# Optimization experiments

Measured on AMD Instinct MI355X. Metric: run time of the kernel, lower is better.

## Reference

```python
import jax, jax.numpy as jnp
import numpy as np

N, IN, HID, OUT, HEADS, E = 50000, 256, 128, 128, 2, 800000
NEG_SLOPE = 0.2


def gat_conv(x, edge_src, edge_dst, W, att_src, att_dst, bias):
    # x: [N, F_in]; W: [F_in, H*C]; att_*: [H, C]; bias: [C]
    n = x.shape[0]
    H, C = att_src.shape
    xl = (x @ W).reshape(n, H, C)                       # [N, H, C]
    a_src = jnp.sum(xl * att_src, axis=-1)              # [N, H]
    a_dst = jnp.sum(xl * att_dst, axis=-1)              # [N, H]
    e = jax.nn.leaky_relu(a_src[edge_src] + a_dst[edge_dst], NEG_SLOPE)  # [E+N, H]
    e_max = jax.ops.segment_max(e, edge_dst, num_segments=n)            # [N, H]
    e = jnp.exp(e - e_max[edge_dst])
    denom = jax.ops.segment_sum(e, edge_dst, num_segments=n)            # [N, H]
    alpha = e / (denom[edge_dst] + 1e-16)                               # [E+N, H]
    msg = xl[edge_src] * alpha[:, :, None]                              # [E+N, H, C]
    out = jax.ops.segment_sum(msg, edge_dst, num_segments=n)            # [N, H, C]
    return out.mean(axis=1) + bias                                      # concat=False: head mean


def setup_inputs() -> dict:
    key = jax.random.key(0)
    ks = jax.random.split(key, 12)
    x = jax.random.normal(ks[0], (N, IN), dtype=jnp.float32)
    edge_index = jax.random.randint(ks[1], (2, E), 0, N, dtype=jnp.int64)
    s = 0.1
    W0 = jax.random.normal(ks[2], (IN, HEADS * HID), dtype=jnp.float32) * s
    att_src0 = jax.random.normal(ks[3], (HEADS, HID), dtype=jnp.float32) * s
    att_dst0 = jax.random.normal(ks[4], (HEADS, HID), dtype=jnp.float32) * s
    bias0 = jnp.zeros((HID,), dtype=jnp.float32)
    W1 = jax.random.normal(ks[5], (HID, HEADS * HID), dtype=jnp.float32) * s
    att_src1 = jax.random.normal(ks[6], (HEADS, HID), dtype=jnp.float32) * s
    att_dst1 = jax.random.normal(ks[7], (HEADS, HID), dtype=jnp.float32) * s
    bias1 = jnp.zeros((HID,), dtype=jnp.float32)
    proj_w = jax.random.normal(ks[8], (HID, OUT), dtype=jnp.float32) * s
    proj_b = jnp.zeros((OUT,), dtype=jnp.float32)
    return {"x": x, "edge_index": edge_index,
            "W0": W0, "att_src0": att_src0, "att_dst0": att_dst0, "bias0": bias0,
            "W1": W1, "att_src1": att_src1, "att_dst1": att_dst1, "bias1": bias1,
            "proj_w": proj_w, "proj_b": proj_b}


def reference(x, edge_index, W0, att_src0, att_dst0, bias0, W1, att_src1, att_dst1, bias1, proj_w, proj_b):
    n = x.shape[0]
    loops = jnp.arange(n, dtype=edge_index.dtype)
    # PyG GATConv default add_self_loops=True
    src = jnp.concatenate([edge_index[0], loops])
    dst = jnp.concatenate([edge_index[1], loops])
    h = gat_conv(x, src, dst, W0, att_src0, att_dst0, bias0)
    h = jax.nn.gelu(h, approximate=False)
    h = gat_conv(h, src, dst, W1, att_src1, att_dst1, bias1)
    h = jax.nn.gelu(h, approximate=False)
    return h @ proj_w + proj_b
```

## Files before the change

### kernel.cpp

```cpp
#include <hip/hip_runtime.h>
#include <math.h>


#define NEG_SLOPE 0.2f

typedef __attribute__((ext_vector_type(8))) short bf16x8;
typedef __attribute__((ext_vector_type(8))) ushort u16x8;
typedef __attribute__((ext_vector_type(4))) float f32x4;

__device__ __forceinline__ void split_f32(float x, ushort& h, ushort& l)
{
    unsigned b = __float_as_uint(x);
    h = (ushort)(b >> 16);
    float xh = __uint_as_float(b & 0xffff0000u);
    l = (ushort)(__float_as_uint(x - xh) >> 16);
}

__device__ __forceinline__ ushort f32_to_bf16_rne(float x)
{
    unsigned u = __float_as_uint(x);
    return (ushort)((u + 0x7fffu + ((u >> 16) & 1u)) >> 16);
}

__device__ __forceinline__ float bf16_to_f32(ushort u)
{
    return __uint_as_float(((unsigned)u) << 16);
}

__device__ __forceinline__ float lrelu(float x)
{
    return x > 0.f ? x : NEG_SLOPE * x;
}

__device__ __forceinline__ float gelu_exact(float x)
{
    return 0.5f * x * (1.0f + erff(x * 0.7071067811865476f));
}

__global__ __launch_bounds__(256)
void split_all_w(const float* __restrict__ W0, const float* __restrict__ W1,
                 const float* __restrict__ PW,
                 ushort* __restrict__ w0h, ushort* __restrict__ w0l,
                 ushort* __restrict__ w1h, ushort* __restrict__ w1l,
                 ushort* __restrict__ pwh, ushort* __restrict__ pwl)
{
    int t = blockIdx.x * 256 + threadIdx.x;
    ushort h, l;
    if (t < 65536) {
        int k = t >> 8, n = t & 255;
        split_f32(W0[t], h, l);
        w0h[n * 256 + k] = h; w0l[n * 256 + k] = l;
    } else if (t < 65536 + 32768) {
        int u = t - 65536;
        int k = u >> 8, n = u & 255;
        split_f32(W1[u], h, l);
        w1h[n * 128 + k] = h; w1l[n * 128 + k] = l;
    } else if (t < 65536 + 32768 + 16384) {
        int u = t - 65536 - 32768;
        int k = u >> 7, n = u & 127;
        split_f32(PW[u], h, l);
        pwh[n * 128 + k] = h; pwl[n * 128 + k] = l;
    }
}

__global__ __launch_bounds__(256)
void watt_prep_kernel(const float* __restrict__ W,
                      const float* __restrict__ att_s,
                      const float* __restrict__ att_d,
                      float* __restrict__ watt,
                      int C, int Nout)
{
    const int k = blockIdx.x;
    const int t = threadIdx.x;
    const int h = t >> 7, c = t & 127;
    const int lane = t & 63, wid = t >> 6;

    float ps = 0.f, pd = 0.f;
    if (c < C) {
        const float w = W[(size_t)k * Nout + h * C + c];
        ps = w * att_s[h * C + c];
        pd = w * att_d[h * C + c];
    }
#pragma unroll
    for (int off = 1; off < 64; off <<= 1) {
        ps += __shfl_xor(ps, off, 64);
        pd += __shfl_xor(pd, off, 64);
    }
    __shared__ float sm[4][2];
    if (lane == 0) { sm[wid][0] = ps; sm[wid][1] = pd; }
    __syncthreads();
    if (t == 0) {
        watt[k * 4 + 0] = sm[0][0] + sm[1][0];
        watt[k * 4 + 1] = sm[2][0] + sm[3][0];
        watt[k * 4 + 2] = sm[0][1] + sm[1][1];
        watt[k * 4 + 3] = sm[2][1] + sm[3][1];
    }
}

__global__ __launch_bounds__(256)
void attn_matvec_kernel(const float* __restrict__ X,
                        const float* __restrict__ watt,
                        float* __restrict__ a_s, float* __restrict__ a_d,
                        int n, int K)
{
    const int wave = threadIdx.x >> 6;
    const int lane = threadIdx.x & 63;
    const int v = blockIdx.x * 4 + wave;
    if (v >= n) return;

    float s0 = 0.f, s1 = 0.f, d0 = 0.f, d1 = 0.f;
    const int k0 = lane << 2;
    if (k0 < K) {
        const float4 xv = *(const float4*)(X + (size_t)v * K + k0);
        const float x4[4] = {xv.x, xv.y, xv.z, xv.w};
#pragma unroll
        for (int i = 0; i < 4; ++i) {
            const float4 wv = *(const float4*)(watt + (k0 + i) * 4);
            s0 += x4[i] * wv.x;
            s1 += x4[i] * wv.y;
            d0 += x4[i] * wv.z;
            d1 += x4[i] * wv.w;
        }
    }
#pragma unroll
    for (int off = 1; off < 64; off <<= 1) {
        s0 += __shfl_xor(s0, off, 64);
        s1 += __shfl_xor(s1, off, 64);
        d0 += __shfl_xor(d0, off, 64);
        d1 += __shfl_xor(d1, off, 64);
    }
    if (lane == 0) {
        *(float2*)(a_s + (size_t)v * 2) = make_float2(s0, s1);
        *(float2*)(a_d + (size_t)v * 2) = make_float2(d0, d1);
    }
}

template<int BN, bool SPLITA>
__global__ __launch_bounds__(512)
void mfma_gemm3(const float* __restrict__ Af,
                const ushort* __restrict__ Aio,
                const ushort* __restrict__ Bth, const ushort* __restrict__ Btl,
                const float* __restrict__ bias,
                float* __restrict__ Cf, ushort* __restrict__ Cb,
                int M, int K)
{
    constexpr int NF = BN / 64;
    __shared__ ushort Ah[4][128][8];
    __shared__ ushort Al[4][128][8];
    __shared__ ushort Bh[4][BN][8];
    __shared__ ushort Bl[4][BN][8];

    const int tid = threadIdx.x;
    const int r0 = blockIdx.x * 128;
    const int w = tid >> 6, lane = tid & 63;
    const int wr = (w & 1) * 64;
    const int wc = (w >> 1) * (BN / 4);
    const int lr = lane & 15, kb = lane >> 4;

    const int arow = tid >> 2;
    const int apl = tid & 3;

    f32x4 acc[4][NF] = {};

    for (int kk = 0; kk < K; kk += 32) {
        {
            const int row = r0 + arow;
            u16x8 h0 = {}, l0 = {};
            if (row < M) {
                if constexpr (SPLITA) {
                    const float* p = Af + (size_t)row * K + kk + apl * 8;
                    float4 v0 = *(const float4*)(p);
                    float4 v1 = *(const float4*)(p + 4);
                    float va[8] = {v0.x, v0.y, v0.z, v0.w, v1.x, v1.y, v1.z, v1.w};
#pragma unroll
                    for (int i = 0; i < 8; ++i) {
                        ushort hh_, ll_;
                        split_f32(va[i], hh_, ll_);
                        h0[i] = hh_; l0[i] = ll_;
                    }
                } else {
                    const ushort* p = Aio + (size_t)row * (2 * K) + kk + apl * 8;
                    h0 = *(const u16x8*)(p);
                    l0 = *(const u16x8*)(p + K);
                }
            }
            *(u16x8*)&Ah[apl][arow][0] = h0;
            *(u16x8*)&Al[apl][arow][0] = l0;
        }
        if constexpr (BN == 256) {
            const int col = tid >> 1, half = tid & 1;
            const ushort* ph = Bth + (size_t)col * K + kk + half * 16;
            const ushort* pl = Btl + (size_t)col * K + kk + half * 16;
            *(u16x8*)&Bh[half * 2 + 0][col][0] = *(const u16x8*)(ph);
            *(u16x8*)&Bh[half * 2 + 1][col][0] = *(const u16x8*)(ph + 8);
            *(u16x8*)&Bl[half * 2 + 0][col][0] = *(const u16x8*)(pl);
            *(u16x8*)&Bl[half * 2 + 1][col][0] = *(const u16x8*)(pl + 8);
        } else {
            const int col = tid >> 2, pl = tid & 3;
            *(u16x8*)&Bh[pl][col][0] = *(const u16x8*)(Bth + (size_t)col * K + kk + pl * 8);
            *(u16x8*)&Bl[pl][col][0] = *(const u16x8*)(Btl + (size_t)col * K + kk + pl * 8);
        }
        __syncthreads();

        bf16x8 ah[4], al[4];
#pragma unroll
        for (int m = 0; m < 4; ++m) {
            ah[m] = *(const bf16x8*)&Ah[kb][wr + m * 16 + lr][0];
            al[m] = *(const bf16x8*)&Al[kb][wr + m * 16 + lr][0];
        }
#pragma unroll
        for (int n = 0; n < NF; ++n) {
            const bf16x8 bh = *(const bf16x8*)&Bh[kb][wc + n * 16 + lr][0];
            const bf16x8 bl = *(const bf16x8*)&Bl[kb][wc + n * 16 + lr][0];
#pragma unroll
            for (int m = 0; m < 4; ++m) {
                acc[m][n] = __builtin_amdgcn_mfma_f32_16x16x32_bf16(ah[m], bh, acc[m][n], 0, 0, 0);
                acc[m][n] = __builtin_amdgcn_mfma_f32_16x16x32_bf16(ah[m], bl, acc[m][n], 0, 0, 0);
                acc[m][n] = __builtin_amdgcn_mfma_f32_16x16x32_bf16(al[m], bh, acc[m][n], 0, 0, 0);
            }
        }
        __syncthreads();
    }

#pragma unroll
    for (int n = 0; n < NF; ++n) {
        const int col = wc + n * 16 + lr;
        const float bv = bias ? bias[col] : 0.f;
#pragma unroll
        for (int m = 0; m < 4; ++m) {
            const int rowb = r0 + wr + m * 16 + kb * 4;
#pragma unroll
            for (int j = 0; j < 4; ++j) {
                const int row = rowb + j;
                if (row < M) {
                    const float val = acc[m][n][j] + bv;
                    if (Cf) Cf[(size_t)row * BN + col] = val;
                    if (Cb) Cb[(size_t)row * BN + col] = f32_to_bf16_rne(val);
                }
            }
        }
    }
}

__global__ __launch_bounds__(256)
void edge_alpha_kernel(const float* __restrict__ a_s,
                       const float* __restrict__ a_d,
                       const int* __restrict__ rowptr,
                       const int* __restrict__ esrc,
                       float* __restrict__ walpha,
                       float* __restrict__ nodeP,
                       int n)
{
    const int wave = threadIdx.x >> 6;
    const int lane = threadIdx.x & 63;
    const int v = blockIdx.x * 4 + wave;
    if (v >= n) return;
    const int h = lane >> 5;
    const int j0 = lane & 31;

    const float adv = a_d[v * 2 + h];
    const float e0 = lrelu(a_s[v * 2 + h] + adv);
    const int beg = rowptr[v], end = rowptr[v + 1];

    float m = e0;
    for (int i = beg + j0; i < end; i += 32) {
        const int src = esrc[i];
        m = fmaxf(m, lrelu(a_s[src * 2 + h] + adv));
    }
#pragma unroll
    for (int off = 1; off < 32; off <<= 1)
        m = fmaxf(m, __shfl_xor(m, off, 64));

    float ssum = (j0 == 0) ? __expf(e0 - m) : 0.f;
    for (int i = beg + j0; i < end; i += 32) {
        const int src = esrc[i];
        const float wgt = __expf(lrelu(a_s[src * 2 + h] + adv) - m);
        walpha[(size_t)i * 2 + h] = wgt;
        ssum += wgt;
    }
#pragma unroll
    for (int off = 1; off < 32; off <<= 1)
        ssum += __shfl_xor(ssum, off, 64);

    if (j0 == 0) {
        float2 p;
        p.x = __expf(e0 - m);
        p.y = 1.0f / (ssum + 1e-16f);
        *(float2*)(nodeP + (size_t)v * 4 + h * 2) = p;
    }
}

__global__ __launch_bounds__(256)
void gat_gather_kernel(const ushort* __restrict__ xlb,
                       const int* __restrict__ rowptr,
                       const int* __restrict__ esrc,
                       const float* __restrict__ walpha,
                       const float* __restrict__ nodeP,
                       const float* __restrict__ bias,
                       const float* __restrict__ watt,
                       float* __restrict__ a_s, float* __restrict__ a_d,
                       ushort* __restrict__ outio,
                       int n)
{
    const int wave = threadIdx.x >> 6;
    const int lane = threadIdx.x & 63;
    const int v = blockIdx.x * 4 + wave;
    if (v >= n) return;
    const int h = lane >> 5;
    const int j0 = lane & 31;
    const int c4 = j0 << 2;

    const float2 p = *(const float2*)(nodeP + (size_t)v * 4 + h * 2);
    const ushort4 xv4 = *(const ushort4*)(xlb + (size_t)v * 256 + (lane << 2));
    float4 acc0, acc1;
    acc0.x = p.x * bf16_to_f32(xv4.x);
    acc0.y = p.x * bf16_to_f32(xv4.y);
    acc0.z = p.x * bf16_to_f32(xv4.z);
    acc0.w = p.x * bf16_to_f32(xv4.w);
    acc1 = make_float4(0.f, 0.f, 0.f, 0.f);

    const int beg = rowptr[v], end = rowptr[v + 1];
    for (int i = beg; i < end; i += 32) {
        const int cnt = min(32, end - i);
        int myidx = 0;
        float myw = 0.f;
        if (j0 < cnt) {
            myidx = esrc[i + j0];
            myw = walpha[(size_t)(i + j0) * 2 + h];
        }
#pragma unroll 2
        for (int j = 0; j < cnt; ++j) {
            const int src = __builtin_amdgcn_readlane(myidx, j);
            const float wgt = __shfl(myw, j, 32);
            const ushort4 xs4 = *(const ushort4*)(xlb + (size_t)src * 256 + (lane << 2));
            if (j & 1) {
                acc1.x += wgt * bf16_to_f32(xs4.x);
                acc1.y += wgt * bf16_to_f32(xs4.y);
                acc1.z += wgt * bf16_to_f32(xs4.z);
                acc1.w += wgt * bf16_to_f32(xs4.w);
            } else {
                acc0.x += wgt * bf16_to_f32(xs4.x);
                acc0.y += wgt * bf16_to_f32(xs4.y);
                acc0.z += wgt * bf16_to_f32(xs4.z);
                acc0.w += wgt * bf16_to_f32(xs4.w);
            }
        }
    }

    float4 r;
    r.x = (acc0.x + acc1.x) * p.y;
    r.y = (acc0.y + acc1.y) * p.y;
    r.z = (acc0.z + acc1.z) * p.y;
    r.w = (acc0.w + acc1.w) * p.y;
    float4 o;
    o.x = 0.5f * (r.x + __shfl_xor(r.x, 32, 64));
    o.y = 0.5f * (r.y + __shfl_xor(r.y, 32, 64));
    o.z = 0.5f * (r.z + __shfl_xor(r.z, 32, 64));
    o.w = 0.5f * (r.w + __shfl_xor(r.w, 32, 64));

    const float4 bb = *(const float4*)(bias + c4);
    o.x = gelu_exact(o.x + bb.x);
    o.y = gelu_exact(o.y + bb.y);
    o.z = gelu_exact(o.z + bb.z);
    o.w = gelu_exact(o.w + bb.w);

    if (watt) {
        const float ov[4] = {o.x, o.y, o.z, o.w};
        float s0 = 0.f, s1 = 0.f, d0 = 0.f, d1 = 0.f;
#pragma unroll
        for (int i = 0; i < 4; ++i) {
            const float4 wv = *(const float4*)(watt + (c4 + i) * 4);
            s0 += ov[i] * wv.x;
            s1 += ov[i] * wv.y;
            d0 += ov[i] * wv.z;
            d1 += ov[i] * wv.w;
        }
#pragma unroll
        for (int off = 1; off < 64; off <<= 1) {
            s0 += __shfl_xor(s0, off, 64);
            s1 += __shfl_xor(s1, off, 64);
            d0 += __shfl_xor(d0, off, 64);
            d1 += __shfl_xor(d1, off, 64);
        }
        if (lane == 0) {
            *(float2*)(a_s + (size_t)v * 2) = make_float2(0.5f * s0, 0.5f * s1);
            *(float2*)(a_d + (size_t)v * 2) = make_float2(0.5f * d0, 0.5f * d1);
        }
    }

    ushort4 st;
    ushort hh_, ll_;
    split_f32(o.x, hh_, ll_); st.x = (lane < 32) ? hh_ : ll_;
    split_f32(o.y, hh_, ll_); st.y = (lane < 32) ? hh_ : ll_;
    split_f32(o.z, hh_, ll_); st.z = (lane < 32) ? hh_ : ll_;
    split_f32(o.w, hh_, ll_); st.w = (lane < 32) ? hh_ : ll_;
    *(ushort4*)(outio + (size_t)v * 256 + (lane << 2)) = st;
}

__global__ __launch_bounds__(256)
void hist_kernel(const int* __restrict__ ei, int* __restrict__ cnt, int E)
{
    int e = blockIdx.x * 256 + threadIdx.x;
    if (e < E) atomicAdd(&cnt[ei[E + e]], 1);
}

__global__ __launch_bounds__(256)
void blocksum_kernel(const int* __restrict__ cnt, int* __restrict__ bsum, int n)
{
    __shared__ int sm[256];
    const int t = threadIdx.x;
    const int i = blockIdx.x * 256 + t;
    sm[t] = (i < n) ? cnt[i] : 0;
    __syncthreads();
#pragma unroll
    for (int off = 1; off < 256; off <<= 1) {
        int u = (t >= off) ? sm[t - off] : 0;
        __syncthreads();
        sm[t] += u;
        __syncthreads();
    }
    if (t == 255) bsum[blockIdx.x] = sm[255];
}

__global__ __launch_bounds__(256)
void scan_bsum_kernel(int* __restrict__ bsum, int nb, int* __restrict__ ptr, int n)
{
    __shared__ int sm[256];
    const int t = threadIdx.x;
    const int v = (t < nb) ? bsum[t] : 0;
    sm[t] = v;
    __syncthreads();
#pragma unroll
    for (int off = 1; off < 256; off <<= 1) {
        int u = (t >= off) ? sm[t - off] : 0;
        __syncthreads();
        sm[t] += u;
        __syncthreads();
    }
    if (t < nb) bsum[t] = sm[t] - v;
    if (t == 255) ptr[n] = sm[255];
}

__global__ __launch_bounds__(256)
void scan_out_kernel(const int* __restrict__ cnt, const int* __restrict__ bsum,
                     int* __restrict__ ptr, int* __restrict__ pcur, int n)
{
    __shared__ int sm[256];
    const int t = threadIdx.x;
    const int i = blockIdx.x * 256 + t;
    const int v = (i < n) ? cnt[i] : 0;
    sm[t] = v;
    __syncthreads();
#pragma unroll
    for (int off = 1; off < 256; off <<= 1) {
        int u = (t >= off) ? sm[t - off] : 0;
        __syncthreads();
        sm[t] += u;
        __syncthreads();
    }
    if (i < n) {
        const int val = bsum[blockIdx.x] + sm[t] - v;
        ptr[i] = val;
        pcur[i] = val;
    }
}

__global__ __launch_bounds__(256)
void scatter_kernel(const int* __restrict__ ei, int* __restrict__ pcur,
                    int* __restrict__ esrc, int E)
{
    int e = blockIdx.x * 256 + threadIdx.x;
    if (e < E) {
        int dst = ei[E + e];
        int src = ei[e];
        int pos = atomicAdd(&pcur[dst], 1);
        esrc[pos] = src;
    }
}

extern "C" void kernel_launch(void* const* d_in, const int* in_sizes, int n_in,
                              void* d_out, int out_size, void* d_ws, size_t ws_size,
                              hipStream_t stream)
{
    const float* x       = (const float*)d_in[0];
    const int*   ei      = (const int*)d_in[1];
    const float* W0      = (const float*)d_in[2];
    const float* att_s0  = (const float*)d_in[3];
    const float* att_d0  = (const float*)d_in[4];
    const float* b0      = (const float*)d_in[5];
    const float* W1      = (const float*)d_in[6];
    const float* att_s1  = (const float*)d_in[7];
    const float* att_d1  = (const float*)d_in[8];
    const float* b1      = (const float*)d_in[9];
    const float* pw      = (const float*)d_in[10];
    const float* pb      = (const float*)d_in[11];

    const int N = in_sizes[0] / 256;
    const int E = in_sizes[1] / 2;
    const int NB = (N + 255) / 256;

    ushort* xlb = (ushort*)d_ws;
    ushort* hio = xlb + (size_t)N * 256;
    float*  a_s = (float*)(hio + (size_t)N * 256);
    float*  a_d = a_s + (size_t)N * 2;
    float*  wal = a_d + (size_t)N * 2;
    float*  ndp = wal + (size_t)E * 2;
    float*  wt0 = ndp + (size_t)N * 4;
    float*  wt1 = wt0 + 256 * 4;
    int*    cnt = (int*)(wt1 + 128 * 4);
    int*    ptr = cnt + N;
    int*    pcur= ptr + (N + 1);
    int*    bsm = pcur + N;
    int*    esr = bsm + 256;
    ushort* w0h = (ushort*)(esr + E);
    ushort* w0l = w0h + 256 * 256;
    ushort* w1h = w0l + 256 * 256;
    ushort* w1l = w1h + 256 * 128;
    ushort* pwh = w1l + 256 * 128;
    ushort* pwl = pwh + 128 * 128;

    const int ablk = (N + 3) / 4;
    const int eblk = (E + 255) / 256;
    const int gblk = (N + 127) / 128;

    split_all_w<<<(65536 + 32768 + 16384 + 255) / 256, 256, 0, stream>>>(
        W0, W1, pw, w0h, w0l, w1h, w1l, pwh, pwl);
    watt_prep_kernel<<<256, 256, 0, stream>>>(W0, att_s0, att_d0, wt0, 128, 256);
    watt_prep_kernel<<<128, 256, 0, stream>>>(W1, att_s1, att_d1, wt1, 128, 256);

    hipMemsetAsync(cnt, 0, (size_t)N * sizeof(int), stream);
    hist_kernel<<<eblk, 256, 0, stream>>>(ei, cnt, E);
    blocksum_kernel<<<NB, 256, 0, stream>>>(cnt, bsm, N);
    scan_bsum_kernel<<<1, 256, 0, stream>>>(bsm, NB, ptr, N);
    scan_out_kernel<<<NB, 256, 0, stream>>>(cnt, bsm, ptr, pcur, N);
    scatter_kernel<<<eblk, 256, 0, stream>>>(ei, pcur, esr, E);

    mfma_gemm3<256, true><<<gblk, 512, 0, stream>>>(
        x, nullptr, w0h, w0l, nullptr, nullptr, xlb, N, 256);
    attn_matvec_kernel<<<ablk, 256, 0, stream>>>(x, wt0, a_s, a_d, N, 256);
    edge_alpha_kernel<<<ablk, 256, 0, stream>>>(a_s, a_d, ptr, esr, wal, ndp, N);
    gat_gather_kernel<<<ablk, 256, 0, stream>>>(
        xlb, ptr, esr, wal, ndp, b0, wt1, a_s, a_d, hio, N);

    mfma_gemm3<256, false><<<gblk, 512, 0, stream>>>(
        nullptr, hio, w1h, w1l, nullptr, nullptr, xlb, N, 128);
    edge_alpha_kernel<<<ablk, 256, 0, stream>>>(a_s, a_d, ptr, esr, wal, ndp, N);
    gat_gather_kernel<<<ablk, 256, 0, stream>>>(
        xlb, ptr, esr, wal, ndp, b1, nullptr, nullptr, nullptr, hio, N);

    mfma_gemm3<128, false><<<gblk, 512, 0, stream>>>(
        nullptr, hio, pwh, pwl, pb, (float*)d_out, nullptr, N, 128);
}
```

Measured before the change: 382.7 us.

## Fuse edge softmax into gather kernel and merge weight prep kernels

```diff
diff --git a/kernel.cpp b/kernel.cpp
--- a/kernel.cpp
+++ b/kernel.cpp
@@ -38,49 +38,48 @@
 }
 
 __global__ __launch_bounds__(256)
-void split_all_w(const float* __restrict__ W0, const float* __restrict__ W1,
+void prep_kernel(const float* __restrict__ W0, const float* __restrict__ W1,
                  const float* __restrict__ PW,
+                 const float* __restrict__ as0, const float* __restrict__ ad0,
+                 const float* __restrict__ as1, const float* __restrict__ ad1,
                  ushort* __restrict__ w0h, ushort* __restrict__ w0l,
                  ushort* __restrict__ w1h, ushort* __restrict__ w1l,
-                 ushort* __restrict__ pwh, ushort* __restrict__ pwl)
-{
-    int t = blockIdx.x * 256 + threadIdx.x;
-    ushort h, l;
-    if (t < 65536) {
-        int k = t >> 8, n = t & 255;
-        split_f32(W0[t], h, l);
-        w0h[n * 256 + k] = h; w0l[n * 256 + k] = l;
-    } else if (t < 65536 + 32768) {
-        int u = t - 65536;
-        int k = u >> 8, n = u & 255;
-        split_f32(W1[u], h, l);
-        w1h[n * 128 + k] = h; w1l[n * 128 + k] = l;
-    } else if (t < 65536 + 32768 + 16384) {
-        int u = t - 65536 - 32768;
-        int k = u >> 7, n = u & 127;
-        split_f32(PW[u], h, l);
-        pwh[n * 128 + k] = h; pwl[n * 128 + k] = l;
-    }
-}
-
-__global__ __launch_bounds__(256)
-void watt_prep_kernel(const float* __restrict__ W,
-                      const float* __restrict__ att_s,
-                      const float* __restrict__ att_d,
-                      float* __restrict__ watt,
-                      int C, int Nout)
-{
-    const int k = blockIdx.x;
+                 ushort* __restrict__ pwh, ushort* __restrict__ pwl,
+                 float* __restrict__ wt0, float* __restrict__ wt1)
+{
+    const int blk = blockIdx.x;
+    if (blk < 448) {
+        int t = blk * 256 + threadIdx.x;
+        ushort h, l;
+        if (t < 65536) {
+            int k = t >> 8, n = t & 255;
+            split_f32(W0[t], h, l);
+            w0h[n * 256 + k] = h; w0l[n * 256 + k] = l;
+        } else if (t < 65536 + 32768) {
+            int u = t - 65536;
+            int k = u >> 8, n = u & 255;
+            split_f32(W1[u], h, l);
+            w1h[n * 128 + k] = h; w1l[n * 128 + k] = l;
+        } else {
+            int u = t - 65536 - 32768;
+            int k = u >> 7, n = u & 127;
+            split_f32(PW[u], h, l);
+            pwh[n * 128 + k] = h; pwl[n * 128 + k] = l;
+        }
+        return;
+    }
+    const float *W, *as_, *ad_;
+    float* wt;
+    int k;
+    if (blk < 704) { W = W0; as_ = as0; ad_ = ad0; wt = wt0; k = blk - 448; }
+    else           { W = W1; as_ = as1; ad_ = ad1; wt = wt1; k = blk - 704; }
+
     const int t = threadIdx.x;
     const int h = t >> 7, c = t & 127;
     const int lane = t & 63, wid = t >> 6;
-
-    float ps = 0.f, pd = 0.f;
-    if (c < C) {
-        const float w = W[(size_t)k * Nout + h * C + c];
-        ps = w * att_s[h * C + c];
-        pd = w * att_d[h * C + c];
-    }
+    const float w = W[(size_t)k * 256 + h * 128 + c];
+    float ps = w * as_[h * 128 + c];
+    float pd = w * ad_[h * 128 + c];
 #pragma unroll
     for (int off = 1; off < 64; off <<= 1) {
         ps += __shfl_xor(ps, off, 64);
@@ -90,10 +89,10 @@
     if (lane == 0) { sm[wid][0] = ps; sm[wid][1] = pd; }
     __syncthreads();
     if (t == 0) {
-        watt[k * 4 + 0] = sm[0][0] + sm[1][0];
-        watt[k * 4 + 1] = sm[2][0] + sm[3][0];
-        watt[k * 4 + 2] = sm[0][1] + sm[1][1];
-        watt[k * 4 + 3] = sm[2][1] + sm[3][1];
+        wt[k * 4 + 0] = sm[0][0] + sm[1][0];
+        wt[k * 4 + 1] = sm[2][0] + sm[3][0];
+        wt[k * 4 + 2] = sm[0][1] + sm[1][1];
+        wt[k * 4 + 3] = sm[2][1] + sm[3][1];
     }
 }
 
@@ -243,62 +242,14 @@
 }
 
 __global__ __launch_bounds__(256)
-void edge_alpha_kernel(const float* __restrict__ a_s,
-                       const float* __restrict__ a_d,
-                       const int* __restrict__ rowptr,
-                       const int* __restrict__ esrc,
-                       float* __restrict__ walpha,
-                       float* __restrict__ nodeP,
-                       int n)
-{
-    const int wave = threadIdx.x >> 6;
-    const int lane = threadIdx.x & 63;
-    const int v = blockIdx.x * 4 + wave;
-    if (v >= n) return;
-    const int h = lane >> 5;
-    const int j0 = lane & 31;
-
-    const float adv = a_d[v * 2 + h];
-    const float e0 = lrelu(a_s[v * 2 + h] + adv);
-    const int beg = rowptr[v], end = rowptr[v + 1];
-
-    float m = e0;
-    for (int i = beg + j0; i < end; i += 32) {
-        const int src = esrc[i];
-        m = fmaxf(m, lrelu(a_s[src * 2 + h] + adv));
-    }
-#pragma unroll
-    for (int off = 1; off < 32; off <<= 1)
-        m = fmaxf(m, __shfl_xor(m, off, 64));
-
-    float ssum = (j0 == 0) ? __expf(e0 - m) : 0.f;
-    for (int i = beg + j0; i < end; i += 32) {
-        const int src = esrc[i];
-        const float wgt = __expf(lrelu(a_s[src * 2 + h] + adv) - m);
-        walpha[(size_t)i * 2 + h] = wgt;
-        ssum += wgt;
-    }
-#pragma unroll
-    for (int off = 1; off < 32; off <<= 1)
-        ssum += __shfl_xor(ssum, off, 64);
-
-    if (j0 == 0) {
-        float2 p;
-        p.x = __expf(e0 - m);
-        p.y = 1.0f / (ssum + 1e-16f);
-        *(float2*)(nodeP + (size_t)v * 4 + h * 2) = p;
-    }
-}
-
-__global__ __launch_bounds__(256)
 void gat_gather_kernel(const ushort* __restrict__ xlb,
                        const int* __restrict__ rowptr,
                        const int* __restrict__ esrc,
-                       const float* __restrict__ walpha,
-                       const float* __restrict__ nodeP,
+                       const float* __restrict__ a_si,
+                       const float* __restrict__ a_di,
                        const float* __restrict__ bias,
                        const float* __restrict__ watt,
-                       float* __restrict__ a_s, float* __restrict__ a_d,
+                       float* __restrict__ a_so, float* __restrict__ a_do,
                        ushort* __restrict__ outio,
                        int n)
 {
@@ -310,14 +261,17 @@
     const int j0 = lane & 31;
     const int c4 = j0 << 2;
 
-    const float2 p = *(const float2*)(nodeP + (size_t)v * 4 + h * 2);
+    const float adv = a_di[v * 2 + h];
+    const float wself = __expf(lrelu(a_si[v * 2 + h] + adv));
+
     const ushort4 xv4 = *(const ushort4*)(xlb + (size_t)v * 256 + (lane << 2));
     float4 acc0, acc1;
-    acc0.x = p.x * bf16_to_f32(xv4.x);
-    acc0.y = p.x * bf16_to_f32(xv4.y);
-    acc0.z = p.x * bf16_to_f32(xv4.z);
-    acc0.w = p.x * bf16_to_f32(xv4.w);
+    acc0.x = wself * bf16_to_f32(xv4.x);
+    acc0.y = wself * bf16_to_f32(xv4.y);
+    acc0.z = wself * bf16_to_f32(xv4.z);
+    acc0.w = wself * bf16_to_f32(xv4.w);
     acc1 = make_float4(0.f, 0.f, 0.f, 0.f);
+    float ssum = (j0 == 0) ? wself : 0.f;
 
     const int beg = rowptr[v], end = rowptr[v + 1];
     for (int i = beg; i < end; i += 32) {
@@ -326,8 +280,9 @@
         float myw = 0.f;
         if (j0 < cnt) {
             myidx = esrc[i + j0];
-            myw = walpha[(size_t)(i + j0) * 2 + h];
-        }
+            myw = __expf(lrelu(a_si[myidx * 2 + h] + adv));
+        }
+        ssum += myw;
 #pragma unroll 2
         for (int j = 0; j < cnt; ++j) {
             const int src = __builtin_amdgcn_readlane(myidx, j);
@@ -347,11 +302,16 @@
         }
     }
 
+#pragma unroll
+    for (int off = 1; off < 32; off <<= 1)
+        ssum += __shfl_xor(ssum, off, 64);
+    const float inv = 1.0f / (ssum + 1e-16f);
+
     float4 r;
-    r.x = (acc0.x + acc1.x) * p.y;
-    r.y = (acc0.y + acc1.y) * p.y;
-    r.z = (acc0.z + acc1.z) * p.y;
-    r.w = (acc0.w + acc1.w) * p.y;
+    r.x = (acc0.x + acc1.x) * inv;
+    r.y = (acc0.y + acc1.y) * inv;
+    r.z = (acc0.z + acc1.z) * inv;
+    r.w = (acc0.w + acc1.w) * inv;
     float4 o;
     o.x = 0.5f * (r.x + __shfl_xor(r.x, 32, 64));
     o.y = 0.5f * (r.y + __shfl_xor(r.y, 32, 64));
@@ -383,8 +343,8 @@
             d1 += __shfl_xor(d1, off, 64);
         }
         if (lane == 0) {
-            *(float2*)(a_s + (size_t)v * 2) = make_float2(0.5f * s0, 0.5f * s1);
-            *(float2*)(a_d + (size_t)v * 2) = make_float2(0.5f * d0, 0.5f * d1);
+            *(float2*)(a_so + (size_t)v * 2) = make_float2(0.5f * s0, 0.5f * s1);
+            *(float2*)(a_do + (size_t)v * 2) = make_float2(0.5f * d0, 0.5f * d1);
         }
     }
 
@@ -499,34 +459,33 @@
     const int E = in_sizes[1] / 2;
     const int NB = (N + 255) / 256;
 
-    ushort* xlb = (ushort*)d_ws;
-    ushort* hio = xlb + (size_t)N * 256;
-    float*  a_s = (float*)(hio + (size_t)N * 256);
-    float*  a_d = a_s + (size_t)N * 2;
-    float*  wal = a_d + (size_t)N * 2;
-    float*  ndp = wal + (size_t)E * 2;
-    float*  wt0 = ndp + (size_t)N * 4;
-    float*  wt1 = wt0 + 256 * 4;
-    int*    cnt = (int*)(wt1 + 128 * 4);
-    int*    ptr = cnt + N;
-    int*    pcur= ptr + (N + 1);
-    int*    bsm = pcur + N;
-    int*    esr = bsm + 256;
-    ushort* w0h = (ushort*)(esr + E);
-    ushort* w0l = w0h + 256 * 256;
-    ushort* w1h = w0l + 256 * 256;
-    ushort* w1l = w1h + 256 * 128;
-    ushort* pwh = w1l + 256 * 128;
-    ushort* pwl = pwh + 128 * 128;
+    ushort* xlb  = (ushort*)d_ws;
+    ushort* hio  = xlb + (size_t)N * 256;
+    float*  a_s  = (float*)(hio + (size_t)N * 256);
+    float*  a_d  = a_s + (size_t)N * 2;
+    float*  a_s2 = a_d + (size_t)N * 2;
+    float*  a_d2 = a_s2 + (size_t)N * 2;
+    float*  wt0  = a_d2 + (size_t)N * 2;
+    float*  wt1  = wt0 + 256 * 4;
+    int*    cnt  = (int*)(wt1 + 128 * 4);
+    int*    ptr  = cnt + N;
+    int*    pcur = ptr + (N + 1);
+    int*    bsm  = pcur + N;
+    int*    esr  = bsm + 256;
+    ushort* w0h  = (ushort*)(esr + E);
+    ushort* w0l  = w0h + 256 * 256;
+    ushort* w1h  = w0l + 256 * 256;
+    ushort* w1l  = w1h + 256 * 128;
+    ushort* pwh  = w1l + 256 * 128;
+    ushort* pwl  = pwh + 128 * 128;
 
     const int ablk = (N + 3) / 4;
     const int eblk = (E + 255) / 256;
     const int gblk = (N + 127) / 128;
 
-    split_all_w<<<(65536 + 32768 + 16384 + 255) / 256, 256, 0, stream>>>(
-        W0, W1, pw, w0h, w0l, w1h, w1l, pwh, pwl);
-    watt_prep_kernel<<<256, 256, 0, stream>>>(W0, att_s0, att_d0, wt0, 128, 256);
-    watt_prep_kernel<<<128, 256, 0, stream>>>(W1, att_s1, att_d1, wt1, 128, 256);
+    prep_kernel<<<832, 256, 0, stream>>>(
+        W0, W1, pw, att_s0, att_d0, att_s1, att_d1,
+        w0h, w0l, w1h, w1l, pwh, pwl, wt0, wt1);
 
     hipMemsetAsync(cnt, 0, (size_t)N * sizeof(int), stream);
     hist_kernel<<<eblk, 256, 0, stream>>>(ei, cnt, E);
@@ -538,15 +497,13 @@
     mfma_gemm3<256, true><<<gblk, 512, 0, stream>>>(
         x, nullptr, w0h, w0l, nullptr, nullptr, xlb, N, 256);
     attn_matvec_kernel<<<ablk, 256, 0, stream>>>(x, wt0, a_s, a_d, N, 256);
-    edge_alpha_kernel<<<ablk, 256, 0, stream>>>(a_s, a_d, ptr, esr, wal, ndp, N);
     gat_gather_kernel<<<ablk, 256, 0, stream>>>(
-        xlb, ptr, esr, wal, ndp, b0, wt1, a_s, a_d, hio, N);
+        xlb, ptr, esr, a_s, a_d, b0, wt1, a_s2, a_d2, hio, N);
 
     mfma_gemm3<256, false><<<gblk, 512, 0, stream>>>(
         nullptr, hio, w1h, w1l, nullptr, nullptr, xlb, N, 128);
-    edge_alpha_kernel<<<ablk, 256, 0, stream>>>(a_s, a_d, ptr, esr, wal, ndp, N);
     gat_gather_kernel<<<ablk, 256, 0, stream>>>(
-        xlb, ptr, esr, wal, ndp, b1, nullptr, nullptr, nullptr, hio, N);
+        xlb, ptr, esr, a_s2, a_d2, b1, nullptr, nullptr, nullptr, hio, N);
 
     mfma_gemm3<128, false><<<gblk, 512, 0, stream>>>(
         nullptr, hio, pwh, pwl, pb, (float*)d_out, nullptr, N, 128);
```

Result: faster. 354.5 us (-7.4%).
